# Kernel tuning notes

Hardware: AMD Instinct MI355X
Metric: run time of the kernel (lower is better)

Reference implementation:

```python
import jax, jax.numpy as jnp
import numpy as np

N = 100000   # num visited nodes
D = 128      # emb_dim
B = 1024     # num queries (eg_idx groups)
DEG = 256    # edges per query group (fixed, > K so topk always prunes)
E = B * DEG  # 262144 edges
K = 20       # max_attended_edges
RATIO = 0.0  # ratio_update
NEG_SLOPE = 0.01  # LeakyReLU default


def segment_softmax(logits, seg, num_segments):
    m = jax.ops.segment_max(logits, seg, num_segments=num_segments)
    ex = jnp.exp(logits - m[seg])
    s = jax.ops.segment_sum(ex, seg, num_segments=num_segments)
    return ex / s[seg]


def setup_inputs() -> dict:
    key = jax.random.key(0)
    ks = jax.random.split(key, 11)
    node_score = jax.random.uniform(ks[0], (N,), dtype=jnp.float32)
    node_repr = jax.random.normal(ks[1], (N, D), dtype=jnp.float32)
    rel_emb = jax.random.normal(ks[2], (E, D), dtype=jnp.float32)
    q_src_emb = jax.random.normal(ks[3], (B, D), dtype=jnp.float32)
    q_rel_emb = jax.random.normal(ks[4], (B, D), dtype=jnp.float32)
    # G3: Linear(4D, 4D, bias=False), init normal std sqrt(2/dim_in)
    Wq = jax.random.normal(ks[5], (4 * D, 4 * D), dtype=jnp.float32) * np.sqrt(2.0 / (4 * D))
    Wk = jax.random.normal(ks[6], (4 * D, 4 * D), dtype=jnp.float32) * np.sqrt(2.0 / (4 * D))
    # linear_between_steps: Linear(D, D) xavier
    W_lin = jax.random.normal(ks[7], (D, D), dtype=jnp.float32) * np.sqrt(2.0 / (2 * D))
    b_lin = jnp.zeros((D,), dtype=jnp.float32)
    # edges: [E, 8]; col0 = eg_idx (sorted, fixed DEG per group), col6 = vi, col7 = vj
    eg = jnp.repeat(jnp.arange(B, dtype=jnp.int32), DEG)
    vi = jax.random.randint(ks[8], (E,), 0, N, dtype=jnp.int32)
    vj = jax.random.randint(ks[9], (E,), 0, N, dtype=jnp.int32)
    z = jnp.zeros((E,), dtype=jnp.int32)
    edges = jnp.stack([eg, z, z, z, z, z, vi, vj], axis=1)
    return {
        "node_score": node_score, "node_repr": node_repr, "rel_emb": rel_emb,
        "q_src_emb": q_src_emb, "q_rel_emb": q_rel_emb,
        "Wq": Wq, "Wk": Wk, "W_lin": W_lin, "b_lin": b_lin, "edges": edges,
    }


def reference(node_score, node_repr, rel_emb, q_src_emb, q_rel_emb, Wq, Wk, W_lin, b_lin, edges):
    eg = edges[:, 0]
    vi = edges[:, 6]
    vj = edges[:, 7]
    # --- G3 attention score over edges ---
    hvi = node_repr[vi]           # [E, D]
    hvj = node_repr[vj]           # [E, D]
    qst = q_src_emb[eg]           # [E, D]
    qr = q_rel_emb[eg]            # [E, D]
    left = jnp.concatenate([hvi, rel_emb, qst, qr], axis=-1)   # [E, 4D]
    right = jnp.concatenate([hvj, rel_emb, qst, qr], axis=-1)  # [E, 4D]
    logits = jnp.sum((left @ Wq.T) * (right @ Wk.T), axis=-1)  # [E]
    # --- segment softmax over source node vi ---
    sm = segment_softmax(logits, vi, N)
    src_score = node_score[vi]
    target_score = sm * src_score
    # --- per-query-group top-k edge pruning (fixed DEG per group) ---
    topk_vals, topk_idx = jax.lax.top_k(target_score.reshape(B, DEG), K)  # [B, K]
    flat_idx = (topk_idx + jnp.arange(B, dtype=topk_idx.dtype)[:, None] * DEG).reshape(-1)  # [B*K]
    p_vi = vi[flat_idx]
    p_vj = vj[flat_idx]
    p_sm = sm[flat_idx]
    p_src = src_score[flat_idx]
    # --- node score aggregation: scatter-sum sm*src_score into target node vj ---
    updated_node_score = jax.ops.segment_sum(p_sm * p_src, p_vj, num_segments=N)
    # --- node representation update (sparse transition + identity fill) ---
    agg = jax.ops.segment_sum((1.0 - RATIO) * p_sm[:, None] * node_repr[p_vj], p_vi, num_segments=N)
    appears = jnp.zeros((N,), dtype=jnp.float32).at[p_vi].set(1.0)
    self_coef = jnp.where(appears > 0, RATIO, 1.0)[:, None]
    updated_repr = agg + self_coef * node_repr
    # --- bypass_forward: LeakyReLU(Linear) ---
    updated_repr = jax.nn.leaky_relu(updated_repr @ W_lin.T + b_lin, NEG_SLOPE)
    return updated_node_score, updated_repr
```

## Files before the change

### kernel.cpp

```cpp
#include <hip/hip_runtime.h>

#define NN 100000
#define BQ 1024
#define EE 262144
#define KTOP 20

typedef unsigned long long ull;
typedef __attribute__((ext_vector_type(8))) short bf16x8;
typedef __attribute__((ext_vector_type(4))) float f32x4;

__device__ __forceinline__ ull enc64(double d) {
  ull u = (ull)__double_as_longlong(d);
  return (u >> 63) ? ~u : (u | 0x8000000000000000ull);
}
__device__ __forceinline__ double dec64(ull u) {
  ull b = (u >> 63) ? (u & 0x7FFFFFFFFFFFFFFFull) : ~u;
  return __longlong_as_double((long long)b);
}

__device__ __forceinline__ unsigned short f2bf(float f) {
  unsigned u = __float_as_uint(f);
  u += 0x7fff + ((u >> 16) & 1);
  return (unsigned short)(u >> 16);
}
__device__ __forceinline__ float bf2f(unsigned short h) {
  return __uint_as_float(((unsigned)h) << 16);
}
__device__ __forceinline__ void cvt8(float4 x, float4 y, bf16x8& hi, bf16x8& lo) {
  float a[8] = {x.x, x.y, x.z, x.w, y.x, y.y, y.z, y.w};
#pragma unroll
  for (int j = 0; j < 8; j++) {
    unsigned short h = f2bf(a[j]);
    float r = a[j] - bf2f(h);
    hi[j] = (short)h;
    lo[j] = (short)f2bf(r);
  }
}

__global__ void k_prep(const int* __restrict__ edges, int4* __restrict__ evi,
                       int* __restrict__ vi32, ull* __restrict__ menc,
                       double* __restrict__ s, float* __restrict__ appears,
                       float* __restrict__ out_score) {
  int i = blockIdx.x * 256 + threadIdx.x;
  int st = gridDim.x * 256;
  for (int e = i; e < EE; e += st) {
    int vi = edges[(size_t)e * 8 + 6];
    evi[e] = make_int4(edges[(size_t)e * 8 + 0], vi, edges[(size_t)e * 8 + 7], 0);
    vi32[e] = vi;
  }
  for (int n = i; n < NN; n += st) {
    menc[n] = 0ull;
    s[n] = 0.0;
    appears[n] = 0.f;
    out_score[n] = 0.f;
  }
}

__global__ void k_matM(const float* __restrict__ Wq, const float* __restrict__ Wk,
                       float* __restrict__ M, float* __restrict__ MT) {
  int x = blockIdx.x;
  int y = blockIdx.y * 256 + threadIdx.x;
  float acc = 0.f;
  for (int a = 0; a < 512; a++)
    acc += Wq[a * 512 + x] * Wk[a * 512 + y];
  M[x * 512 + y] = acc;
  MT[y * 512 + x] = acc;
}

__global__ void k_pack(const float* __restrict__ M, const float* __restrict__ MT,
                       const float* __restrict__ Wl,
                       short* __restrict__ wn_hi, short* __restrict__ wn_lo,
                       short* __restrict__ m11_hi, short* __restrict__ m11_lo,
                       short* __restrict__ wl_hi, short* __restrict__ wl_lo) {
  int idx = blockIdx.x * 256 + threadIdx.x;
  if (idx >= 5 * 16384) return;
  int arr = idx >> 14;
  int j16 = idx & 16383;
  int g = j16 >> 9;
  int l = (j16 >> 3) & 63;
  int jj = j16 & 7;
  int c = (g >> 2) * 16 + (l & 15);
  int k = (g & 3) * 32 + ((l >> 4) << 3) + jj;
  float v;
  short *dh, *dl;
  if (arr == 0)      { v = MT[(size_t)c * 512 + k];               dh = wn_hi;          dl = wn_lo; }
  else if (arr == 1) { v = MT[(size_t)(128 + c) * 512 + k];       dh = wn_hi + 16384;  dl = wn_lo + 16384; }
  else if (arr == 2) { v = M[(size_t)(128 + c) * 512 + k];        dh = wn_hi + 32768;  dl = wn_lo + 32768; }
  else if (arr == 3) { v = MT[(size_t)(128 + c) * 512 + 128 + k]; dh = m11_hi;         dl = m11_lo; }
  else               { v = Wl[(size_t)c * 128 + k];               dh = wl_hi;          dl = wl_lo; }
  unsigned short h = f2bf(v);
  float r = v - bf2f(h);
  dh[j16] = (short)h;
  dl[j16] = (short)f2bf(r);
}

__global__ void k_pq(const float* __restrict__ M, const float* __restrict__ MT,
                     const float* __restrict__ qsA, const float* __restrict__ qrA,
                     float* __restrict__ Qv, double* __restrict__ cq) {
  int b = blockIdx.x, d = threadIdx.x;
  __shared__ float qs[128], qr[128];
  qs[d] = qsA[b * 128 + d];
  qr[d] = qrA[b * 128 + d];
  __syncthreads();
  float uh = 0, ui = 0, ur = 0;
  for (int x = 0; x < 128; x++) {
    float qsx = qs[x], qrx = qr[x];
    uh += qsx * M[(256 + x) * 512 + d]        + qrx * M[(384 + x) * 512 + d];
    ur += qsx * M[(256 + x) * 512 + 128 + d]  + qrx * M[(384 + x) * 512 + 128 + d];
    ui += qsx * MT[(256 + x) * 512 + d]       + qrx * MT[(384 + x) * 512 + d];
    ur += qsx * MT[(256 + x) * 512 + 128 + d] + qrx * MT[(384 + x) * 512 + 128 + d];
  }
  Qv[b * 384 + d]       = uh;
  Qv[b * 384 + 128 + d] = ui;
  Qv[b * 384 + 256 + d] = ur;
  float t1 = 0, t2 = 0;
  for (int y = 0; y < 128; y++) {
    float qsy = qs[y], qry = qr[y];
    t1 += qsy * MT[(256 + y) * 512 + 256 + d] + qry * MT[(384 + y) * 512 + 256 + d];
    t2 += qsy * MT[(256 + y) * 512 + 384 + d] + qry * MT[(384 + y) * 512 + 384 + d];
  }
  float cp = qs[d] * t1 + qr[d] * t2;
  for (int off = 32; off; off >>= 1) cp += __shfl_down(cp, off, 64);
  __shared__ float red[2];
  if ((d & 63) == 0) red[d >> 6] = cp;
  __syncthreads();
  if (d == 0) cq[b] = (double)(red[0] + red[1]);
}

__global__ __launch_bounds__(512) void k_gemm_node(const float* __restrict__ A,
                                                   const short* __restrict__ WT_hi,
                                                   const short* __restrict__ WT_lo,
                                                   float* __restrict__ G,
                                                   float* __restrict__ H1,
                                                   float* __restrict__ J) {
  __shared__ __align__(16) float As[64][132];
  __shared__ __align__(16) short Bh[16384];
  float* Of = (float*)Bh;
  int t = threadIdx.x;
  int row0 = blockIdx.x * 64;
  int w = t >> 6, l = t & 63;
  int rt = w & 3;
  int c0 = (w >> 2) * 4;
#pragma unroll
  for (int i = 0; i < 4; i++) {
    int fi = t + i * 512;
    int r = fi >> 5, c4 = (fi & 31) * 4;
    float4 v = make_float4(0.f, 0.f, 0.f, 0.f);
    if (row0 + r < NN) v = *(const float4*)(A + (size_t)(row0 + r) * 128 + c4);
    *(float4*)&As[r][c4] = v;
    *(bf16x8*)&Bh[fi * 8] = *(const bf16x8*)(WT_hi + fi * 8);
  }
  __syncthreads();
  int rloc = rt * 16 + (l & 15);
  int kq = (l >> 4) * 8;
  for (int panel = 0; panel < 3; panel++) {
    const short* sl = WT_lo + panel * 16384;
    bf16x8 blv[4][4];
#pragma unroll
    for (int cc = 0; cc < 4; cc++)
#pragma unroll
      for (int kt = 0; kt < 4; kt++)
        blv[cc][kt] = *(const bf16x8*)(sl + (((c0 + cc) * 4 + kt) * 64 + l) * 8);
    f32x4 acc[4];
#pragma unroll
    for (int cc = 0; cc < 4; cc++)
#pragma unroll
      for (int j = 0; j < 4; j++) acc[cc][j] = 0.f;
#pragma unroll
    for (int kt = 0; kt < 4; kt++) {
      int kb = kt * 32 + kq;
      float4 x = *(const float4*)&As[rloc][kb];
      float4 y = *(const float4*)&As[rloc][kb + 4];
      bf16x8 ah, al;
      cvt8(x, y, ah, al);
#pragma unroll
      for (int cc = 0; cc < 4; cc++) {
        int off = (((cc + c0) * 4 + kt) * 64 + l) * 8;
        bf16x8 bhv = *(const bf16x8*)&Bh[off];
        acc[cc] = __builtin_amdgcn_mfma_f32_16x16x32_bf16(ah, bhv, acc[cc], 0, 0, 0);
        acc[cc] = __builtin_amdgcn_mfma_f32_16x16x32_bf16(al, bhv, acc[cc], 0, 0, 0);
        acc[cc] = __builtin_amdgcn_mfma_f32_16x16x32_bf16(ah, blv[cc][kt], acc[cc], 0, 0, 0);
      }
    }
    __syncthreads();
#pragma unroll
    for (int cc = 0; cc < 4; cc++) {
      int col = (c0 + cc) * 16 + (l & 15);
#pragma unroll
      for (int reg = 0; reg < 4; reg++)
        Of[(rt * 16 + (l >> 4) * 4 + reg) * 128 + col] = acc[cc][reg];
    }
    __syncthreads();
    float* dst = (panel == 0) ? G : (panel == 1) ? H1 : J;
#pragma unroll
    for (int i = 0; i < 4; i++) {
      int fi = t + i * 512;
      int r = fi >> 5, c4 = (fi & 31) * 4;
      int rr = row0 + r;
      if (rr < NN) *(float4*)&dst[(size_t)rr * 128 + c4] = *(float4*)&Of[r * 128 + c4];
    }
    if (panel < 2) {
      __syncthreads();
      const short* sh = WT_hi + (panel + 1) * 16384;
#pragma unroll
      for (int i = 0; i < 4; i++) {
        int fi = t + i * 512;
        *(bf16x8*)&Bh[fi * 8] = *(const bf16x8*)(sh + fi * 8);
      }
      __syncthreads();
    }
  }
}

__global__ __launch_bounds__(512, 1) void k_edge(const float* __restrict__ rel,
                                                 const short* __restrict__ M11T_hi,
                                                 const short* __restrict__ M11T_lo,
                                                 const int4* __restrict__ evi,
                                                 const float* __restrict__ H1,
                                                 const float* __restrict__ J,
                                                 const float* __restrict__ G,
                                                 const float* __restrict__ nrep,
                                                 const float* __restrict__ Qv,
                                                 const double* __restrict__ cq,
                                                 double* __restrict__ logits,
                                                 ull* __restrict__ menc) {
  __shared__ __align__(16) float Rs[64][132];
  __shared__ __align__(16) short Bh[16384];
  __shared__ float part[4][64];
  __shared__ float dg[64];
  __shared__ float uhs[128], uis[128], urs[128];
  __shared__ double cqs;
  int t = threadIdx.x;
  int e0 = blockIdx.x * 64;
  int eg = e0 >> 8;
  int w = t >> 6, l = t & 63;
  int cq2 = w & 3;
  int rh = w >> 2;
  int gg = t >> 4, ll = t & 15, d = ll * 8;
  int4 edA = evi[e0 + gg * 2];
  int4 edB = evi[e0 + gg * 2 + 1];
  const float* pA1 = H1 + (size_t)edA.y * 128 + d;
  const float* pA2 = J + (size_t)edA.z * 128 + d;
  const float* pB1 = H1 + (size_t)edB.y * 128 + d;
  const float* pB2 = J + (size_t)edB.z * 128 + d;
  float4 Aa0 = *(const float4*)pA1, Aa1 = *(const float4*)(pA1 + 4);
  float4 Ab0 = *(const float4*)pA2, Ab1 = *(const float4*)(pA2 + 4);
  float4 Ba0 = *(const float4*)pB1, Ba1 = *(const float4*)(pB1 + 4);
  float4 Bb0 = *(const float4*)pB2, Bb1 = *(const float4*)(pB2 + 4);
  bf16x8 blv[2][4];
#pragma unroll
  for (int cc = 0; cc < 2; cc++)
#pragma unroll
    for (int kt = 0; kt < 4; kt++)
      blv[cc][kt] = *(const bf16x8*)(M11T_lo + (((cq2 * 2 + cc) * 4 + kt) * 64 + l) * 8);
#pragma unroll
  for (int i = 0; i < 4; i++) {
    int fi = t + i * 512;
    int r = fi >> 5, c4 = (fi & 31) * 4;
    *(float4*)&Rs[r][c4] = *(const float4*)(rel + (size_t)(e0 + r) * 128 + c4);
    *(bf16x8*)&Bh[fi * 8] = *(const bf16x8*)(M11T_hi + fi * 8);
  }
  if (t < 128) {
    uhs[t] = Qv[(size_t)eg * 384 + t];
    uis[t] = Qv[(size_t)eg * 384 + 128 + t];
    urs[t] = Qv[(size_t)eg * 384 + 256 + t];
  }
  if (t == 0) cqs = cq[eg];
  __syncthreads();
  int kq = (l >> 4) * 8;
  int rq4 = (l >> 4) * 4;
#pragma unroll
  for (int rt2 = 0; rt2 < 2; rt2++) {
    int rt = rh * 2 + rt2;
    int rloc = rt * 16 + (l & 15);
    f32x4 acc[2];
#pragma unroll
    for (int cc = 0; cc < 2; cc++)
#pragma unroll
      for (int j = 0; j < 4; j++) acc[cc][j] = 0.f;
#pragma unroll
    for (int kt = 0; kt < 4; kt++) {
      int kb = kt * 32 + kq;
      float4 x = *(const float4*)&Rs[rloc][kb];
      float4 y = *(const float4*)&Rs[rloc][kb + 4];
      bf16x8 ah, al;
      cvt8(x, y, ah, al);
#pragma unroll
      for (int cc = 0; cc < 2; cc++) {
        bf16x8 bhv = *(const bf16x8*)&Bh[(((cq2 * 2 + cc) * 4 + kt) * 64 + l) * 8];
        acc[cc] = __builtin_amdgcn_mfma_f32_16x16x32_bf16(ah, bhv, acc[cc], 0, 0, 0);
        acc[cc] = __builtin_amdgcn_mfma_f32_16x16x32_bf16(al, bhv, acc[cc], 0, 0, 0);
        acc[cc] = __builtin_amdgcn_mfma_f32_16x16x32_bf16(ah, blv[cc][kt], acc[cc], 0, 0, 0);
      }
    }
    float p[4] = {0.f, 0.f, 0.f, 0.f};
#pragma unroll
    for (int cc = 0; cc < 2; cc++) {
      int c = (cq2 * 2 + cc) * 16 + (l & 15);
#pragma unroll
      for (int reg = 0; reg < 4; reg++)
        p[reg] += acc[cc][reg] * Rs[rt * 16 + rq4 + reg][c];
    }
#pragma unroll
    for (int reg = 0; reg < 4; reg++) {
      p[reg] += __shfl_xor(p[reg], 1, 64);
      p[reg] += __shfl_xor(p[reg], 2, 64);
      p[reg] += __shfl_xor(p[reg], 4, 64);
      p[reg] += __shfl_xor(p[reg], 8, 64);
    }
    if ((l & 15) == 0) {
#pragma unroll
      for (int reg = 0; reg < 4; reg++) part[cq2][rt * 16 + rq4 + reg] = p[reg];
    }
  }
  float4 u0 = *(const float4*)&urs[d], u1 = *(const float4*)&urs[d + 4];
  {
    int le = gg * 2;
    float4 r0 = *(const float4*)&Rs[le][d], r1 = *(const float4*)&Rs[le][d + 4];
    float dot = (Aa0.x + Ab0.x + u0.x) * r0.x + (Aa0.y + Ab0.y + u0.y) * r0.y
              + (Aa0.z + Ab0.z + u0.z) * r0.z + (Aa0.w + Ab0.w + u0.w) * r0.w
              + (Aa1.x + Ab1.x + u1.x) * r1.x + (Aa1.y + Ab1.y + u1.y) * r1.y
              + (Aa1.z + Ab1.z + u1.z) * r1.z + (Aa1.w + Ab1.w + u1.w) * r1.w;
    dot += __shfl_xor(dot, 1, 64);
    dot += __shfl_xor(dot, 2, 64);
    dot += __shfl_xor(dot, 4, 64);
    dot += __shfl_xor(dot, 8, 64);
    if (ll == 0) dg[le] = dot;
  }
  {
    int le = gg * 2 + 1;
    float4 r0 = *(const float4*)&Rs[le][d], r1 = *(const float4*)&Rs[le][d + 4];
    float dot = (Ba0.x + Bb0.x + u0.x) * r0.x + (Ba0.y + Bb0.y + u0.y) * r0.y
              + (Ba0.z + Bb0.z + u0.z) * r0.z + (Ba0.w + Bb0.w + u0.w) * r0.w
              + (Ba1.x + Bb1.x + u1.x) * r1.x + (Ba1.y + Bb1.y + u1.y) * r1.y
              + (Ba1.z + Bb1.z + u1.z) * r1.z + (Ba1.w + Bb1.w + u1.w) * r1.w;
    dot += __shfl_xor(dot, 1, 64);
    dot += __shfl_xor(dot, 2, 64);
    dot += __shfl_xor(dot, 4, 64);
    dot += __shfl_xor(dot, 8, 64);
    if (ll == 0) dg[le] = dot;
  }
  const float* gA  = G + (size_t)edA.y * 128 + d;
  const float* iA  = nrep + (size_t)edA.y * 128 + d;
  const float* jA  = nrep + (size_t)edA.z * 128 + d;
  const float* gB  = G + (size_t)edB.y * 128 + d;
  const float* iB  = nrep + (size_t)edB.y * 128 + d;
  const float* jB  = nrep + (size_t)edB.z * 128 + d;
  float4 GA0 = *(const float4*)gA, GA1 = *(const float4*)(gA + 4);
  float4 IA0 = *(const float4*)iA, IA1 = *(const float4*)(iA + 4);
  float4 JA0 = *(const float4*)jA, JA1 = *(const float4*)(jA + 4);
  float4 GB0 = *(const float4*)gB, GB1 = *(const float4*)(gB + 4);
  float4 IB0 = *(const float4*)iB, IB1 = *(const float4*)(iB + 4);
  float4 JB0 = *(const float4*)jB, JB1 = *(const float4*)(jB + 4);
  __syncthreads();
  float4 h0 = *(const float4*)&uhs[d], h1 = *(const float4*)&uhs[d + 4];
  float4 i0 = *(const float4*)&uis[d], i1 = *(const float4*)&uis[d + 4];
  {
    int le = gg * 2;
    float gd = (GA0.x + h0.x) * JA0.x + (GA0.y + h0.y) * JA0.y
             + (GA0.z + h0.z) * JA0.z + (GA0.w + h0.w) * JA0.w
             + (GA1.x + h1.x) * JA1.x + (GA1.y + h1.y) * JA1.y
             + (GA1.z + h1.z) * JA1.z + (GA1.w + h1.w) * JA1.w
             + i0.x * IA0.x + i0.y * IA0.y + i0.z * IA0.z + i0.w * IA0.w
             + i1.x * IA1.x + i1.y * IA1.y + i1.z * IA1.z + i1.w * IA1.w;
    gd += __shfl_xor(gd, 1, 64);
    gd += __shfl_xor(gd, 2, 64);
    gd += __shfl_xor(gd, 4, 64);
    gd += __shfl_xor(gd, 8, 64);
    if (ll == 0) {
      float base = ((part[0][le] + part[1][le]) + (part[2][le] + part[3][le])) + dg[le] + gd;
      double l2 = (double)base + cqs;
      logits[e0 + le] = l2;
      atomicMax(&menc[edA.y], enc64(l2));
    }
  }
  {
    int le = gg * 2 + 1;
    float gd = (GB0.x + h0.x) * JB0.x + (GB0.y + h0.y) * JB0.y
             + (GB0.z + h0.z) * JB0.z + (GB0.w + h0.w) * JB0.w
             + (GB1.x + h1.x) * JB1.x + (GB1.y + h1.y) * JB1.y
             + (GB1.z + h1.z) * JB1.z + (GB1.w + h1.w) * JB1.w
             + i0.x * IB0.x + i0.y * IB0.y + i0.z * IB0.z + i0.w * IB0.w
             + i1.x * IB1.x + i1.y * IB1.y + i1.z * IB1.z + i1.w * IB1.w;
    gd += __shfl_xor(gd, 1, 64);
    gd += __shfl_xor(gd, 2, 64);
    gd += __shfl_xor(gd, 4, 64);
    gd += __shfl_xor(gd, 8, 64);
    if (ll == 0) {
      float base = ((part[0][le] + part[1][le]) + (part[2][le] + part[3][le])) + dg[le] + gd;
      double l2 = (double)base + cqs;
      logits[e0 + le] = l2;
      atomicMax(&menc[edB.y], enc64(l2));
    }
  }
}

__global__ void k_exp(const int* __restrict__ vi32, const ull* __restrict__ menc,
                      const double* __restrict__ logits, double* __restrict__ ex,
                      double* __restrict__ s, float4* __restrict__ agg) {
  int i = blockIdx.x * 256 + threadIdx.x;
  int st = gridDim.x * 256;
  for (int e = i; e < EE; e += st) {
    int vi = vi32[e];
    double m = dec64(menc[vi]);
    double v = exp(logits[e] - m);
    ex[e] = v;
    atomicAdd(&s[vi], v);
  }
  const int n4 = NN * 32;
  for (int n = i; n < n4; n += st) agg[n] = make_float4(0.f, 0.f, 0.f, 0.f);
}

__global__ void k_topk(const double* __restrict__ ex, const double* __restrict__ s,
                       const float* __restrict__ nscore, const int4* __restrict__ evi,
                       const float* __restrict__ nrep, float* __restrict__ out_score,
                       float* __restrict__ agg, float* __restrict__ appears) {
  int b = blockIdx.x, t = threadIdx.x;
  int e = b * 256 + t;
  int vi_t = evi[e].y;
  double v = ex[e] / s[vi_t] * (double)nscore[vi_t];
  __shared__ double cv[80];
  __shared__ int ci[80];
  __shared__ int winners[KTOP];
  int w = t >> 6;
  for (int k = 0; k < KTOP; k++) {
    double bv = v;
    int bi = t;
    for (int off = 32; off; off >>= 1) {
      double ov = __shfl_down(bv, off, 64);
      int oi = __shfl_down(bi, off, 64);
      if (ov > bv || (ov == bv && oi < bi)) { bv = ov; bi = oi; }
    }
    bi = __shfl(bi, 0, 64);
    if ((t & 63) == 0) { cv[w * KTOP + k] = bv; ci[w * KTOP + k] = bi; }
    if (t == bi) v = -1.0;
  }
  __syncthreads();
  if (t < 64) {
    double v0 = cv[t];
    int i0 = ci[t];
    double v1 = (t < 16) ? cv[64 + t] : -2.0;
    int i1 = (t < 16) ? ci[64 + t] : (1 << 30);
    for (int k = 0; k < KTOP; k++) {
      double bv; int bi;
      if (v1 > v0 || (v1 == v0 && i1 < i0)) { bv = v1; bi = i1; }
      else                                  { bv = v0; bi = i0; }
      for (int off = 32; off; off >>= 1) {
        double ov = __shfl_down(bv, off, 64);
        int oi = __shfl_down(bi, off, 64);
        if (ov > bv || (ov == bv && oi < bi)) { bv = ov; bi = oi; }
      }
      bi = __shfl(bi, 0, 64);
      if (t == 0) winners[k] = bi;
      if (i0 == bi) v0 = -2.0;
      if (i1 == bi) v1 = -2.0;
    }
  }
  __syncthreads();
  for (int k = 0; k < KTOP; k++) {
    int we = b * 256 + winners[k];
    int4 ew = evi[we];
    int vi = ew.y, vj = ew.z;
    double sm = ex[we] / s[vi];
    if (t < 128) {
      atomicAdd(&agg[(size_t)vi * 128 + t], (float)sm * nrep[(size_t)vj * 128 + t]);
    } else if (t == 128) {
      atomicAdd(&out_score[vj], (float)(sm * (double)nscore[vi]));
    } else if (t == 129) {
      appears[vi] = 1.f;
    }
  }
}

__global__ __launch_bounds__(512) void k_final(const float* __restrict__ agg,
                                               const float* __restrict__ appears,
                                               const float* __restrict__ nrep,
                                               const short* __restrict__ Wl_hi,
                                               const short* __restrict__ Wl_lo,
                                               const float* __restrict__ bl,
                                               float* __restrict__ outr) {
  __shared__ __align__(16) float Xs[64][132];
  __shared__ __align__(16) short Bh[16384];
  int t = threadIdx.x;
  int row0 = blockIdx.x * 64;
  int w = t >> 6, l = t & 63;
  int rt = w & 3;
  int c0 = (w >> 2) * 4;
  bf16x8 blv[4][4];
#pragma unroll
  for (int cc = 0; cc < 4; cc++)
#pragma unroll
    for (int kt = 0; kt < 4; kt++)
      blv[cc][kt] = *(const bf16x8*)(Wl_lo + (((c0 + cc) * 4 + kt) * 64 + l) * 8);
#pragma unroll
  for (int i = 0; i < 4; i++) {
    int fi = t + i * 512;
    int r = fi >> 5, c4 = (fi & 31) * 4;
    int rr = row0 + r;
    float4 v = make_float4(0.f, 0.f, 0.f, 0.f);
    if (rr < NN) {
      float4 ag = *(const float4*)(agg + (size_t)rr * 128 + c4);
      float4 h = *(const float4*)(nrep + (size_t)rr * 128 + c4);
      float coef = (appears[rr] > 0.f) ? 0.f : 1.f;
      v.x = ag.x + coef * h.x;
      v.y = ag.y + coef * h.y;
      v.z = ag.z + coef * h.z;
      v.w = ag.w + coef * h.w;
    }
    *(float4*)&Xs[r][c4] = v;
    *(bf16x8*)&Bh[fi * 8] = *(const bf16x8*)(Wl_hi + fi * 8);
  }
  __syncthreads();
  int rloc = rt * 16 + (l & 15);
  int kq = (l >> 4) * 8;
  f32x4 acc[4];
#pragma unroll
  for (int cc = 0; cc < 4; cc++)
#pragma unroll
    for (int j = 0; j < 4; j++) acc[cc][j] = 0.f;
#pragma unroll
  for (int kt = 0; kt < 4; kt++) {
    int kb = kt * 32 + kq;
    float4 x = *(const float4*)&Xs[rloc][kb];
    float4 y = *(const float4*)&Xs[rloc][kb + 4];
    bf16x8 ah, al;
    cvt8(x, y, ah, al);
#pragma unroll
    for (int cc = 0; cc < 4; cc++) {
      int off = (((c0 + cc) * 4 + kt) * 64 + l) * 8;
      bf16x8 bhv = *(const bf16x8*)&Bh[off];
      acc[cc] = __builtin_amdgcn_mfma_f32_16x16x32_bf16(ah, bhv, acc[cc], 0, 0, 0);
      acc[cc] = __builtin_amdgcn_mfma_f32_16x16x32_bf16(al, bhv, acc[cc], 0, 0, 0);
      acc[cc] = __builtin_amdgcn_mfma_f32_16x16x32_bf16(ah, blv[cc][kt], acc[cc], 0, 0, 0);
    }
  }
  __syncthreads();
#pragma unroll
  for (int cc = 0; cc < 4; cc++) {
    int col = (c0 + cc) * 16 + (l & 15);
#pragma unroll
    for (int reg = 0; reg < 4; reg++)
      Xs[rt * 16 + (l >> 4) * 4 + reg][col] = acc[cc][reg];
  }
  __syncthreads();
#pragma unroll
  for (int i = 0; i < 4; i++) {
    int fi = t + i * 512;
    int r = fi >> 5, c4 = (fi & 31) * 4;
    int rr = row0 + r;
    if (rr < NN) {
      float4 v = *(float4*)&Xs[r][c4];
      float4 bb = *(const float4*)&bl[c4];
      float4 o;
      o.x = v.x + bb.x; o.x = (o.x > 0.f) ? o.x : 0.01f * o.x;
      o.y = v.y + bb.y; o.y = (o.y > 0.f) ? o.y : 0.01f * o.y;
      o.z = v.z + bb.z; o.z = (o.z > 0.f) ? o.z : 0.01f * o.z;
      o.w = v.w + bb.w; o.w = (o.w > 0.f) ? o.w : 0.01f * o.w;
      *(float4*)&outr[(size_t)rr * 128 + c4] = o;
    }
  }
}

extern "C" void kernel_launch(void* const* d_in, const int* in_sizes, int n_in,
                              void* d_out, int out_size, void* d_ws, size_t ws_size,
                              hipStream_t stream) {
  const float* node_score = (const float*)d_in[0];
  const float* node_repr  = (const float*)d_in[1];
  const float* rel_emb    = (const float*)d_in[2];
  const float* q_src      = (const float*)d_in[3];
  const float* q_rel      = (const float*)d_in[4];
  const float* Wq         = (const float*)d_in[5];
  const float* Wk         = (const float*)d_in[6];
  const float* W_lin      = (const float*)d_in[7];
  const float* b_lin      = (const float*)d_in[8];
  const int*   edges      = (const int*)d_in[9];

  char* ws = (char*)d_ws;
  size_t off = 0;
  auto carve = [&](size_t bytes) -> void* {
    void* p = ws + off;
    off += (bytes + 255) & ~(size_t)255;
    return p;
  };
  float*  M      = (float*)carve(512 * 512 * 4);
  float*  MT     = (float*)carve(512 * 512 * 4);
  short*  wn_hi  = (short*)carve(3 * 16384 * 2);
  short*  wn_lo  = (short*)carve(3 * 16384 * 2);
  short*  m11_hi = (short*)carve(16384 * 2);
  short*  m11_lo = (short*)carve(16384 * 2);
  short*  wl_hi  = (short*)carve(16384 * 2);
  short*  wl_lo  = (short*)carve(16384 * 2);
  float*  Qv     = (float*)carve((size_t)BQ * 384 * 4);
  double* cq     = (double*)carve((size_t)BQ * 8);
  double* logits = (double*)carve((size_t)EE * 8);
  ull*    menc   = (ull*)carve((size_t)NN * 8);
  double* s      = (double*)carve((size_t)NN * 8);
  double* ex     = (double*)carve((size_t)EE * 8);
  float*  appears= (float*)carve((size_t)NN * 4);
  int4*   evi    = (int4*)carve((size_t)EE * 16);
  int*    vi32   = (int*)carve((size_t)EE * 4);
  float*  G      = (float*)carve((size_t)NN * 128 * 4);
  float*  H1     = (float*)carve((size_t)NN * 128 * 4);
  float*  J      = (float*)carve((size_t)NN * 128 * 4);
  float*  agg    = G;

  float* out_score = (float*)d_out;
  float* out_repr  = (float*)d_out + NN;

  k_prep<<<1024, 256, 0, stream>>>(edges, evi, vi32, menc, s, appears, out_score);
  k_matM<<<dim3(512, 2), 256, 0, stream>>>(Wq, Wk, M, MT);
  k_pack<<<320, 256, 0, stream>>>(M, MT, W_lin, wn_hi, wn_lo, m11_hi, m11_lo, wl_hi, wl_lo);
  k_pq<<<BQ, 128, 0, stream>>>(M, MT, q_src, q_rel, Qv, cq);
  k_gemm_node<<<1563, 512, 0, stream>>>(node_repr, wn_hi, wn_lo, G, H1, J);
  k_edge<<<4096, 512, 0, stream>>>(rel_emb, m11_hi, m11_lo, evi, H1, J, G, node_repr, Qv, cq, logits, menc);
  k_exp<<<2048, 256, 0, stream>>>(vi32, menc, logits, ex, s, (float4*)agg);
  k_topk<<<BQ, 256, 0, stream>>>(ex, s, node_score, evi, node_repr, out_score, agg, appears);
  k_final<<<1563, 512, 0, stream>>>(agg, appears, node_repr, wl_hi, wl_lo, b_lin, out_repr);
}
```

Before: 369.1 us.

## Interleave per-node G, H1 and node_repr into one 384-wide row for edge gathers

The node GEMM now writes its G and H1 panels plus a copy of node_repr into one interleaved per-node buffer of 384 floats, and J stays separate. The edge kernel gathers everything indexed by vi from this single contiguous row instead of three separate arrays. This is meant to improve locality of the random gathers, since the three vi-indexed reads now land in nearby lines and pages. In exchange the GEMM writes an extra copy of node_repr, and agg now aliases the larger buffer.

After: 456.5 us. 23.7% more time.

```diff
diff --git a/kernel.cpp b/kernel.cpp
--- a/kernel.cpp
+++ b/kernel.cpp
@@ -130,8 +130,7 @@
 __global__ __launch_bounds__(512) void k_gemm_node(const float* __restrict__ A,
                                                    const short* __restrict__ WT_hi,
                                                    const short* __restrict__ WT_lo,
-                                                   float* __restrict__ G,
-                                                   float* __restrict__ H1,
+                                                   float* __restrict__ PV,
                                                    float* __restrict__ J) {
   __shared__ __align__(16) float As[64][132];
   __shared__ __align__(16) short Bh[16384];
@@ -191,13 +190,17 @@
         Of[(rt * 16 + (l >> 4) * 4 + reg) * 128 + col] = acc[cc][reg];
     }
     __syncthreads();
-    float* dst = (panel == 0) ? G : (panel == 1) ? H1 : J;
 #pragma unroll
     for (int i = 0; i < 4; i++) {
       int fi = t + i * 512;
       int r = fi >> 5, c4 = (fi & 31) * 4;
       int rr = row0 + r;
-      if (rr < NN) *(float4*)&dst[(size_t)rr * 128 + c4] = *(float4*)&Of[r * 128 + c4];
+      if (rr < NN) {
+        float4 v = *(float4*)&Of[r * 128 + c4];
+        if (panel == 0)      *(float4*)&PV[(size_t)rr * 384 + c4] = v;
+        else if (panel == 1) *(float4*)&PV[(size_t)rr * 384 + 128 + c4] = v;
+        else                 *(float4*)&J[(size_t)rr * 128 + c4] = v;
+      }
     }
     if (panel < 2) {
       __syncthreads();
@@ -210,15 +213,21 @@
       __syncthreads();
     }
   }
+#pragma unroll
+  for (int i = 0; i < 4; i++) {
+    int fi = t + i * 512;
+    int r = fi >> 5, c4 = (fi & 31) * 4;
+    int rr = row0 + r;
+    if (rr < NN) *(float4*)&PV[(size_t)rr * 384 + 256 + c4] = *(float4*)&As[r][c4];
+  }
 }
 
 __global__ __launch_bounds__(512, 1) void k_edge(const float* __restrict__ rel,
                                                  const short* __restrict__ M11T_hi,
                                                  const short* __restrict__ M11T_lo,
                                                  const int4* __restrict__ evi,
-                                                 const float* __restrict__ H1,
+                                                 const float* __restrict__ PV,
                                                  const float* __restrict__ J,
-                                                 const float* __restrict__ G,
                                                  const float* __restrict__ nrep,
                                                  const float* __restrict__ Qv,
                                                  const double* __restrict__ cq,
@@ -239,14 +248,14 @@
   int gg = t >> 4, ll = t & 15, d = ll * 8;
   int4 edA = evi[e0 + gg * 2];
   int4 edB = evi[e0 + gg * 2 + 1];
-  const float* pA1 = H1 + (size_t)edA.y * 128 + d;
+  const float* pvA = PV + (size_t)edA.y * 384;
+  const float* pvB = PV + (size_t)edB.y * 384;
   const float* pA2 = J + (size_t)edA.z * 128 + d;
-  const float* pB1 = H1 + (size_t)edB.y * 128 + d;
   const float* pB2 = J + (size_t)edB.z * 128 + d;
-  float4 Aa0 = *(const float4*)pA1, Aa1 = *(const float4*)(pA1 + 4);
-  float4 Ab0 = *(const float4*)pA2, Ab1 = *(const float4*)(pA2 + 4);
-  float4 Ba0 = *(const float4*)pB1, Ba1 = *(const float4*)(pB1 + 4);
-  float4 Bb0 = *(const float4*)pB2, Bb1 = *(const float4*)(pB2 + 4);
+  float4 Aa0 = *(const float4*)(pvA + 128 + d), Aa1 = *(const float4*)(pvA + 132 + d);
+  float4 Ab0 = *(const float4*)pA2,             Ab1 = *(const float4*)(pA2 + 4);
+  float4 Ba0 = *(const float4*)(pvB + 128 + d), Ba1 = *(const float4*)(pvB + 132 + d);
+  float4 Bb0 = *(const float4*)pB2,             Bb1 = *(const float4*)(pB2 + 4);
   bf16x8 blv[2][4];
 #pragma unroll
   for (int cc = 0; cc < 2; cc++)
@@ -340,17 +349,13 @@
     dot += __shfl_xor(dot, 8, 64);
     if (ll == 0) dg[le] = dot;
   }
-  const float* gA  = G + (size_t)edA.y * 128 + d;
-  const float* iA  = nrep + (size_t)edA.y * 128 + d;
-  const float* jA  = nrep + (size_t)edA.z * 128 + d;
-  const float* gB  = G + (size_t)edB.y * 128 + d;
-  const float* iB  = nrep + (size_t)edB.y * 128 + d;
-  const float* jB  = nrep + (size_t)edB.z * 128 + d;
-  float4 GA0 = *(const float4*)gA, GA1 = *(const float4*)(gA + 4);
-  float4 IA0 = *(const float4*)iA, IA1 = *(const float4*)(iA + 4);
+  float4 GA0 = *(const float4*)(pvA + d),       GA1 = *(const float4*)(pvA + 4 + d);
+  float4 IA0 = *(const float4*)(pvA + 256 + d), IA1 = *(const float4*)(pvA + 260 + d);
+  const float* jA = nrep + (size_t)edA.z * 128 + d;
   float4 JA0 = *(const float4*)jA, JA1 = *(const float4*)(jA + 4);
-  float4 GB0 = *(const float4*)gB, GB1 = *(const float4*)(gB + 4);
-  float4 IB0 = *(const float4*)iB, IB1 = *(const float4*)(iB + 4);
+  float4 GB0 = *(const float4*)(pvB + d),       GB1 = *(const float4*)(pvB + 4 + d);
+  float4 IB0 = *(const float4*)(pvB + 256 + d), IB1 = *(const float4*)(pvB + 260 + d);
+  const float* jB = nrep + (size_t)edB.z * 128 + d;
   float4 JB0 = *(const float4*)jB, JB1 = *(const float4*)(jB + 4);
   __syncthreads();
   float4 h0 = *(const float4*)&uhs[d], h1 = *(const float4*)&uhs[d + 4];
@@ -599,10 +604,9 @@
   float*  appears= (float*)carve((size_t)NN * 4);
   int4*   evi    = (int4*)carve((size_t)EE * 16);
   int*    vi32   = (int*)carve((size_t)EE * 4);
-  float*  G      = (float*)carve((size_t)NN * 128 * 4);
-  float*  H1     = (float*)carve((size_t)NN * 128 * 4);
+  float*  PV     = (float*)carve((size_t)NN * 384 * 4);
   float*  J      = (float*)carve((size_t)NN * 128 * 4);
-  float*  agg    = G;
+  float*  agg    = PV;
 
   float* out_score = (float*)d_out;
   float* out_repr  = (float*)d_out + NN;
@@ -611,8 +615,8 @@
   k_matM<<<dim3(512, 2), 256, 0, stream>>>(Wq, Wk, M, MT);
   k_pack<<<320, 256, 0, stream>>>(M, MT, W_lin, wn_hi, wn_lo, m11_hi, m11_lo, wl_hi, wl_lo);
   k_pq<<<BQ, 128, 0, stream>>>(M, MT, q_src, q_rel, Qv, cq);
-  k_gemm_node<<<1563, 512, 0, stream>>>(node_repr, wn_hi, wn_lo, G, H1, J);
-  k_edge<<<4096, 512, 0, stream>>>(rel_emb, m11_hi, m11_lo, evi, H1, J, G, node_repr, Qv, cq, logits, menc);
+  k_gemm_node<<<1563, 512, 0, stream>>>(node_repr, wn_hi, wn_lo, PV, J);
+  k_edge<<<4096, 512, 0, stream>>>(rel_emb, m11_hi, m11_lo, evi, PV, J, node_repr, Qv, cq, logits, menc);
   k_exp<<<2048, 256, 0, stream>>>(vi32, menc, logits, ex, s, (float4*)agg);
   k_topk<<<BQ, 256, 0, stream>>>(ex, s, node_score, evi, node_repr, out_score, agg, appears);
   k_final<<<1563, 512, 0, stream>>>(agg, appears, node_repr, wl_hi, wl_lo, b_lin, out_repr);
```
